# Kernel tuning notes

Hardware: AMD Instinct MI355X
Metric: run time of the kernel (lower is better)

The kernel has to match this reference:

```python
import jax, jax.numpy as jnp
import numpy as np

H = W = 64      # patch grid (shape)
WS = 8          # window_size
SHIFT = 4       # shift_size (SW-MSA)
HEAD_DIM = 32
N = WS * WS     # tokens per window


def _rel_position_index(ws):
    coords = np.stack(np.meshgrid(np.arange(ws), np.arange(ws), indexing='ij'))  # (2, ws, ws)
    cf = coords.reshape(2, -1)
    rel = cf[:, :, None] - cf[:, None, :]            # (2, N, N)
    rel = rel.transpose(1, 2, 0).astype(np.int64)    # (N, N, 2)
    rel[..., 0] += ws - 1
    rel[..., 1] += ws - 1
    rel[..., 0] *= 2 * ws - 1
    return (rel[..., 0] + rel[..., 1]).astype(np.int32)  # (N, N), values in [0,(2ws-1)^2)


def _shift_mask(h, w, ws, shift):
    # Swin cyclic-shift attention mask: (num_windows, N, N) with 0 / -100
    img = np.zeros((h, w), dtype=np.float32)
    cnt = 0
    slices = (slice(0, -ws), slice(-ws, -shift), slice(-shift, None))
    for hs in slices:
        for ws_ in slices:
            img[hs, ws_] = cnt
            cnt += 1
    win = img.reshape(h // ws, ws, w // ws, ws).transpose(0, 2, 1, 3).reshape(-1, ws * ws)
    diff = win[:, None, :] - win[:, :, None]
    return np.where(diff != 0, np.float32(-100.0), np.float32(0.0))


def setup_inputs() -> dict:
    key = jax.random.key(0)
    ks = jax.random.split(key, 6)
    dim = 384
    B = 32
    sd = 1.0 / np.sqrt(dim)
    return {
        'x': jax.random.normal(ks[0], (B, H * W, dim), jnp.float32),
        'qkv_w': jax.random.normal(ks[1], (dim, 3 * dim), jnp.float32) * sd,
        'qkv_b': jnp.zeros((3 * dim,), jnp.float32),
        'proj_w': jax.random.normal(ks[2], (dim, dim), jnp.float32) * sd,
        'proj_b': jnp.zeros((dim,), jnp.float32),
        'bias_table': jax.random.normal(ks[3], ((2 * WS - 1) ** 2, dim // HEAD_DIM), jnp.float32) * 0.02,
        'rel_index': jnp.asarray(_rel_position_index(WS)),
    }


def reference(x, qkv_w, qkv_b, proj_w, proj_b, bias_table, rel_index):
    B, L, C = x.shape
    heads = C // HEAD_DIM
    scale = HEAD_DIM ** -0.5
    nh, nw = H // WS, W // WS

    xg = x.reshape(B, H, W, C)
    if SHIFT > 0:
        xg = jnp.roll(xg, shift=(-SHIFT, -SHIFT), axis=(1, 2))

    # window partition -> (B*nWin, N, C)
    xw = xg.reshape(B, nh, WS, nw, WS, C).transpose(0, 1, 3, 2, 4, 5).reshape(B * nh * nw, N, C)

    qkv = xw @ qkv_w + qkv_b                              # (Bw, N, 3C)
    q, k, v = jnp.split(qkv, 3, axis=-1)
    def heads_first(t):
        return t.reshape(-1, N, heads, HEAD_DIM).transpose(0, 2, 1, 3)  # (Bw, h, N, d)
    q, k, v = heads_first(q), heads_first(k), heads_first(v)

    attn = jnp.einsum('bhnd,bhmd->bhnm', q * scale, k)    # (Bw, h, N, N)
    bias = bias_table[rel_index]                          # (N, N, h)
    attn = attn + bias.transpose(2, 0, 1)[None]

    if SHIFT > 0:
        mask = jnp.asarray(_shift_mask(H, W, WS, SHIFT))  # (nWin, N, N), trace-time constant
        attn = attn.reshape(B, nh * nw, heads, N, N) + mask[None, :, None]
        attn = attn.reshape(B * nh * nw, heads, N, N)

    attn = jax.nn.softmax(attn, axis=-1)
    out = jnp.einsum('bhnm,bhmd->bhnd', attn, v)          # (Bw, h, N, d)
    out = out.transpose(0, 2, 1, 3).reshape(B * nh * nw, N, C)
    out = out @ proj_w + proj_b

    # window reverse
    out = out.reshape(B, nh, nw, WS, WS, C).transpose(0, 1, 3, 2, 4, 5).reshape(B, H, W, C)
    if SHIFT > 0:
        out = jnp.roll(out, shift=(SHIFT, SHIFT), axis=(1, 2))
    return out.reshape(B, L, C)
```

## Files before the change

### kernel.cpp

```cpp
#include <hip/hip_runtime.h>
#include <hip/hip_bf16.h>

#define CDIM 384
#define NQKV 1152
#define HEADS 12
#define SHIFT_ 4
#define SCALE_Q 0.17677669529663687f

typedef __attribute__((ext_vector_type(8))) short bf16x8;
typedef __attribute__((ext_vector_type(4))) float f32x4;
typedef __attribute__((ext_vector_type(4))) float float4_t;
typedef __attribute__((ext_vector_type(4))) unsigned u32x4;
typedef __attribute__((ext_vector_type(2))) unsigned u32x2;

__device__ inline short f2bf(float f) {
    union { float f; unsigned u; } v; v.f = f;
    unsigned r = v.u + 0x7FFFu + ((v.u >> 16) & 1u);
    return (short)(r >> 16);
}

__device__ inline unsigned cvtpk(float lo, float hi) {
    unsigned r;
    asm("v_cvt_pk_bf16_f32 %0, %1, %2" : "=v"(r) : "v"(lo), "v"(hi));
    return r;
}

__device__ inline bf16x8 mk8(unsigned w0, unsigned w1, unsigned w2, unsigned w3) {
    u32x4 t = {w0, w1, w2, w3};
    return __builtin_bit_cast(bf16x8, t);
}

__device__ inline bf16x8 pack8(float4_t a, float4_t b) {
    return mk8(cvtpk(a[0], a[1]), cvtpk(a[2], a[3]),
               cvtpk(b[0], b[1]), cvtpk(b[2], b[3]));
}

__device__ inline bf16x8 regroup(unsigned p0, unsigned p1, unsigned p2,
                                 unsigned p3, int lane) {
    int lhi = (lane >> 4) & 3;
    int s0 = (lane & 15) + ((lhi & 1) ? 32 : 0);
    int s1 = s0 + 16;
    unsigned a0 = __shfl(p0, s0), b0 = __shfl(p2, s0);
    unsigned a1 = __shfl(p1, s0), b1 = __shfl(p3, s0);
    unsigned a2 = __shfl(p0, s1), b2 = __shfl(p2, s1);
    unsigned a3 = __shfl(p1, s1), b3 = __shfl(p3, s1);
    bool hi = lhi >= 2;
    return mk8(hi ? b0 : a0, hi ? b1 : a1, hi ? b2 : a2, hi ? b3 : a3);
}

__device__ inline void gl16(const short* g, const short* l) {
    __builtin_amdgcn_global_load_lds((const __attribute__((address_space(1))) void*)g,
                                     (__attribute__((address_space(3))) void*)l, 16, 0, 0);
}

__device__ inline int invswz(int c) {
    int b2 = (c >> 2) & 1, b3 = (c >> 3) & 1, b4 = (c >> 4) & 1;
    return (c & ~7) | ((b2 ^ b4) << 2) | (((((c >> 1) & 1)) ^ b3) << 1) | ((c & 1) ^ b2 ^ b4);
}

__device__ inline int region_id(int wIdx, int tok) {
    int gh = ((wIdx >> 3) << 3) + (tok >> 3);
    int gw = (wIdx & 7) * 8 + (tok & 7);
    int rh = gh < 56 ? 0 : (gh < 60 ? 1 : 2);
    int rw = gw < 56 ? 0 : (gw < 60 ? 1 : 2);
    return rh * 3 + rw;
}

__device__ inline int crow(int row) { return row * 136 + (row >> 3) * 8; }

__device__ inline size_t xrow(int mg) {
    int tok = mg & 63, win = mg >> 6;
    int b = win >> 6, wIdx = win & 63;
    int gh = ((wIdx >> 3) << 3) + (tok >> 3);
    int gw = (wIdx & 7) * 8 + (tok & 7);
    int sh_ = (gh + SHIFT_) & 63, sw_ = (gw + SHIFT_) & 63;
    return (size_t)(b * 4096 + sh_ * 64 + sw_) * CDIM;
}

__global__ void prep_kernel(const float* __restrict__ qkv_w,
                            const float* __restrict__ proj_w,
                            const float* __restrict__ bias_table,
                            const int* __restrict__ rel_index,
                            short* __restrict__ qkvwt,
                            short* __restrict__ projwt,
                            float* __restrict__ biasP) {
    int t = blockIdx.x * 256 + threadIdx.x;
    if (t < NQKV * CDIM) {
        int n = t / CDIM, k = t - n * CDIM;
        qkvwt[t] = f2bf(qkv_w[k * NQKV + n]);
    }
    if (t < CDIM * CDIM) {
        int n = t / CDIM, k = t - n * CDIM;
        projwt[t] = f2bf(proj_w[k * CDIM + n]);
    }
    if (t < HEADS * 16 * 64 * 4) {
        int r = t & 3, lane = (t >> 2) & 63, g = (t >> 8) & 15, h = t >> 12;
        int kt = g >> 2, qt = g & 3;
        int key = kt * 16 + (lane >> 4) * 4 + r;
        int query = qt * 16 + (lane & 15);
        biasP[t] = bias_table[rel_index[query * 64 + key] * HEADS + h];
    }
}

__global__ __launch_bounds__(256) void gemm_qkv(
    const float* __restrict__ x, const short* __restrict__ wt,
    const float* __restrict__ qkv_b, short* __restrict__ qkbuf,
    short* __restrict__ vT)
{
    __shared__ alignas(16) char smemb[40960];
    short* As = (short*)smemb;
    short* Bs = As + 8192;
    short* Cst = (short*)smemb;
    int tid = threadIdx.x;
    int hw = blockIdx.x;
    int lb = (hw & 7) * 1152 + (hw >> 3);
    int bm = lb / 9, bn = lb - bm * 9;
    int m0 = bm * 128, n0 = bn * 128;

    int lane = tid & 63, wv = tid >> 6;
    int c0 = wv * 128 + lane, c1 = c0 + 64;
    const float* Asrc0 = x + xrow(m0 + (c0 >> 2)) + (c0 & 3) * 8;
    const float* Asrc1 = x + xrow(m0 + (c1 >> 2)) + (c1 & 3) * 8;
    short* Aw0 = As + (c0 ^ ((c0 >> 2) & 7)) * 8;
    short* Aw1 = As + (c1 ^ ((c1 >> 2) & 7)) * 8;
    int l0 = invswz(c0), l1 = invswz(c1);
    const short* Bg0 = wt + (size_t)(n0 + (l0 >> 2)) * CDIM + (l0 & 3) * 8;
    const short* Bg1 = wt + (size_t)(n0 + (l1 >> 2)) * CDIM + (l1 & 3) * 8;
    short* Bdst0 = Bs + wv * 1024;
    short* Bdst1 = Bdst0 + 512;

    int wr = wv >> 1, wc = wv & 1;
    int lrow = lane & 15, lhi = lane >> 4;
    int arow = wr * 64 + lrow, brow = wc * 64 + lrow;
    const short* ard = As + ((((arow * 64 + lhi * 16)) ^ ((lrow & 7) << 4)) >> 1);
    const short* brd = Bs + ((((brow * 64 + lhi * 16)) ^ ((lrow & 7) << 4)) >> 1);

    f32x4 zero = {0.f, 0.f, 0.f, 0.f};
    f32x4 acc[4][4];
    #pragma unroll
    for (int i = 0; i < 4; i++)
        #pragma unroll
        for (int j = 0; j < 4; j++) acc[i][j] = zero;

    float4_t sA0[4], sA1[4];
    {
        sA0[0] = *(const float4_t*)(Asrc0);
        sA0[1] = *(const float4_t*)(Asrc0 + 4);
        sA0[2] = *(const float4_t*)(Asrc1);
        sA0[3] = *(const float4_t*)(Asrc1 + 4);
        gl16(Bg0, Bdst0);
        gl16(Bg1, Bdst1);
        gl16(Bg0 + 32, Bdst0 + 4096);
        gl16(Bg1 + 32, Bdst1 + 4096);
        *(bf16x8*)Aw0 = pack8(sA0[0], sA0[1]);
        *(bf16x8*)Aw1 = pack8(sA0[2], sA0[3]);
        sA1[0] = *(const float4_t*)(Asrc0 + 32);
        sA1[1] = *(const float4_t*)(Asrc0 + 36);
        sA1[2] = *(const float4_t*)(Asrc1 + 32);
        sA1[3] = *(const float4_t*)(Asrc1 + 36);
    }
    __builtin_amdgcn_sched_barrier(0);
    asm volatile("s_waitcnt vmcnt(6) lgkmcnt(0)");
    __builtin_amdgcn_s_barrier();
    __builtin_amdgcn_sched_barrier(0);

    #pragma unroll
    for (int ks = 0; ks < 12; ks++) {
        int curA = (ks & 1) * 4096, nxtA = 4096 - curA;
        int curB = (ks % 3) * 4096;
        if (ks < 10) {
            int k2 = (ks + 2) * 32;
            int b2 = ((ks + 2) % 3) * 4096;
            gl16(Bg0 + k2, Bdst0 + b2);
            gl16(Bg1 + k2, Bdst1 + b2);
        }
        if (ks < 11) {
            if ((ks + 1) & 1) {
                *(bf16x8*)(Aw0 + nxtA) = pack8(sA1[0], sA1[1]);
                *(bf16x8*)(Aw1 + nxtA) = pack8(sA1[2], sA1[3]);
            } else {
                *(bf16x8*)(Aw0 + nxtA) = pack8(sA0[0], sA0[1]);
                *(bf16x8*)(Aw1 + nxtA) = pack8(sA0[2], sA0[3]);
            }
        }
        if (ks < 10) {
            int k2 = (ks + 2) * 32;
            if (ks & 1) {
                sA1[0] = *(const float4_t*)(Asrc0 + k2);
                sA1[1] = *(const float4_t*)(Asrc0 + k2 + 4);
                sA1[2] = *(const float4_t*)(Asrc1 + k2);
                sA1[3] = *(const float4_t*)(Asrc1 + k2 + 4);
            } else {
                sA0[0] = *(const float4_t*)(Asrc0 + k2);
                sA0[1] = *(const float4_t*)(Asrc0 + k2 + 4);
                sA0[2] = *(const float4_t*)(Asrc1 + k2);
                sA0[3] = *(const float4_t*)(Asrc1 + k2 + 4);
            }
        }
        bf16x8 af[4], bfr[4];
        #pragma unroll
        for (int t = 0; t < 4; t++) af[t]  = *(const bf16x8*)(ard + curA + t * 512);
        #pragma unroll
        for (int t = 0; t < 4; t++) bfr[t] = *(const bf16x8*)(brd + curB + t * 512);
        __builtin_amdgcn_s_setprio(1);
        #pragma unroll
        for (int i = 0; i < 4; i++)
            #pragma unroll
            for (int j = 0; j < 4; j++)
                acc[i][j] = __builtin_amdgcn_mfma_f32_16x16x32_bf16(af[i], bfr[j], acc[i][j], 0, 0, 0);
        __builtin_amdgcn_s_setprio(0);
        __builtin_amdgcn_sched_barrier(0);
        asm volatile("s_waitcnt vmcnt(6) lgkmcnt(0)");
        __builtin_amdgcn_s_barrier();
        __builtin_amdgcn_sched_barrier(0);
    }
    #pragma unroll
    for (int tj = 0; tj < 4; tj++) {
        int col = wc * 64 + tj * 16 + lrow;
        int cg = n0 + col;
        float bias = qkv_b[cg];
        float sc = (cg < CDIM) ? SCALE_Q : 1.0f;
        #pragma unroll
        for (int ti = 0; ti < 4; ti++) {
            int row0 = wr * 64 + ti * 16 + lhi * 4;
            #pragma unroll
            for (int r = 0; r < 4; r++)
                Cst[crow(row0 + r) + col] = f2bf((acc[ti][tj][r] + bias) * sc);
        }
    }
    __syncthreads();
    if (bn < 6) {
        #pragma unroll
        for (int i = 0; i < 8; i++) {
            int rr = i * 16 + (tid >> 4);
            int cc = (tid & 15) * 8;
            bf16x8 v = *(const bf16x8*)(Cst + crow(rr) + cc);
            __builtin_nontemporal_store(v,
                (bf16x8*)(qkbuf + (size_t)(m0 + rr) * 768 + n0 + cc));
        }
    } else {
        #pragma unroll
        for (int it = 0; it < 8; it++) {
            int t = it * 256 + tid;
            int col = t >> 4, tk8 = t & 15;
            bf16x8 v;
            #pragma unroll
            for (int j = 0; j < 8; j++)
                v[j] = Cst[crow(tk8 * 8 + j) + col];
            int win = bm * 2 + (tk8 >> 3);
            int head = (bn - 6) * 4 + (col >> 5);
            int dim = col & 31;
            __builtin_nontemporal_store(v,
                (bf16x8*)(vT + (((size_t)win * HEADS + head) * 32 + dim) * 64 + (tk8 & 7) * 8));
        }
    }
}

__global__ __launch_bounds__(256) void attn_reg(
    const short* __restrict__ qkbuf, const short* __restrict__ vT,
    const float* __restrict__ biasP, short* __restrict__ attno)
{
    int tid = threadIdx.x;
    int lane = tid & 63, wv = tid >> 6;
    int lrow = lane & 15, lhi = lane >> 4;
    int task = blockIdx.x * 4 + wv;
    int w = task / 12, h = task - w * 12;
    int wIdx = w & 63;
    bool needmask = ((wIdx >> 3) == 7) || ((wIdx & 7) == 7);

    int rq[4], rk[4][4];
    #pragma unroll
    for (int qt = 0; qt < 4; qt++) rq[qt] = region_id(wIdx, qt * 16 + lrow);
    #pragma unroll
    for (int kt = 0; kt < 4; kt++)
        #pragma unroll
        for (int r = 0; r < 4; r++)
            rk[kt][r] = region_id(wIdx, kt * 16 + lhi * 4 + r);

    f32x4 zero = {0.f, 0.f, 0.f, 0.f};
    const short* qbase = qkbuf + (size_t)(w * 64) * 768;

    bf16x8 kf[4];
    #pragma unroll
    for (int kt = 0; kt < 4; kt++)
        kf[kt] = __builtin_nontemporal_load(
            (const bf16x8*)(qbase + (size_t)(kt * 16 + lrow) * 768 + CDIM + h * 32 + lhi * 8));
    bf16x8 pa[4][2];
    #pragma unroll
    for (int qt = 0; qt < 4; qt++) {
        bf16x8 qf = __builtin_nontemporal_load(
            (const bf16x8*)(qbase + (size_t)(qt * 16 + lrow) * 768 + h * 32 + lhi * 8));
        f32x4 st[4];
        __builtin_amdgcn_s_setprio(1);
        #pragma unroll
        for (int kt = 0; kt < 4; kt++)
            st[kt] = __builtin_amdgcn_mfma_f32_16x16x32_bf16(kf[kt], qf, zero, 0, 0, 0);
        __builtin_amdgcn_s_setprio(0);
        float pv[16]; float sum = 0.f;
        #pragma unroll
        for (int kt = 0; kt < 4; kt++) {
            f32x4 bb = *(const f32x4*)(biasP + (((size_t)h * 16 + kt * 4 + qt) * 64 + lane) * 4);
            #pragma unroll
            for (int r = 0; r < 4; r++) {
                float p = __expf(st[kt][r] + bb[r]);
                p = (needmask && (rq[qt] != rk[kt][r])) ? 0.f : p;
                pv[kt * 4 + r] = p; sum += p;
            }
        }
        sum += __shfl_xor(sum, 16);
        sum += __shfl_xor(sum, 32);
        float rcp = 1.0f / sum;
        unsigned a0 = cvtpk(pv[0] * rcp, pv[1] * rcp);
        unsigned a1 = cvtpk(pv[2] * rcp, pv[3] * rcp);
        unsigned a2 = cvtpk(pv[4] * rcp, pv[5] * rcp);
        unsigned a3 = cvtpk(pv[6] * rcp, pv[7] * rcp);
        pa[qt][0] = regroup(a0, a1, a2, a3, lane);
        a0 = cvtpk(pv[8] * rcp,  pv[9] * rcp);
        a1 = cvtpk(pv[10] * rcp, pv[11] * rcp);
        a2 = cvtpk(pv[12] * rcp, pv[13] * rcp);
        a3 = cvtpk(pv[14] * rcp, pv[15] * rcp);
        pa[qt][1] = regroup(a0, a1, a2, a3, lane);
    }
    const short* vb = vT + ((size_t)w * HEADS + h) * 32 * 64;
    bf16x8 vfrag[2][2];
    #pragma unroll
    for (int ks2 = 0; ks2 < 2; ks2++)
        #pragma unroll
        for (int dt = 0; dt < 2; dt++)
            vfrag[ks2][dt] = __builtin_nontemporal_load(
                (const bf16x8*)(vb + (size_t)(dt * 16 + lrow) * 64 + ks2 * 32 + lhi * 8));
    f32x4 ao2[4][2];
    #pragma unroll
    for (int qt = 0; qt < 4; qt++) { ao2[qt][0] = zero; ao2[qt][1] = zero; }
    __builtin_amdgcn_s_setprio(1);
    #pragma unroll
    for (int ks2 = 0; ks2 < 2; ks2++)
        #pragma unroll
        for (int qt = 0; qt < 4; qt++) {
            ao2[qt][0] = __builtin_amdgcn_mfma_f32_16x16x32_bf16(vfrag[ks2][0], pa[qt][ks2], ao2[qt][0], 0, 0, 0);
            ao2[qt][1] = __builtin_amdgcn_mfma_f32_16x16x32_bf16(vfrag[ks2][1], pa[qt][ks2], ao2[qt][1], 0, 0, 0);
        }
    __builtin_amdgcn_s_setprio(0);
    short* abase = attno + (size_t)(w * 64) * CDIM + h * 32 + lhi * 4;
    #pragma unroll
    for (int qt = 0; qt < 4; qt++) {
        int token = qt * 16 + lrow;
        short* p0 = abase + (size_t)token * CDIM;
        u32x2 s0, s1;
        s0[0] = cvtpk(ao2[qt][0][0], ao2[qt][0][1]);
        s0[1] = cvtpk(ao2[qt][0][2], ao2[qt][0][3]);
        s1[0] = cvtpk(ao2[qt][1][0], ao2[qt][1][1]);
        s1[1] = cvtpk(ao2[qt][1][2], ao2[qt][1][3]);
        __builtin_nontemporal_store(s0, (u32x2*)(p0));
        __builtin_nontemporal_store(s1, (u32x2*)(p0 + 16));
    }
}

__global__ __launch_bounds__(256) void gemm_proj(
    const short* __restrict__ a, const short* __restrict__ wt,
    const float* __restrict__ proj_b, float* __restrict__ out)
{
    __shared__ alignas(16) short As[8192];
    __shared__ alignas(16) short Bs[8192];
    int tid = threadIdx.x;
    int hw = blockIdx.x;
    int lb = (hw & 7) * 384 + (hw >> 3);
    int bm = lb / 3, bn = lb - bm * 3;
    int m0 = bm * 128, n0 = bn * 128;

    int lane = tid & 63, wv = tid >> 6;
    int c0 = wv * 128 + lane, c1 = c0 + 64;
    int l0 = invswz(c0), l1 = invswz(c1);
    const short* Ag0 = a + (size_t)(m0 + (l0 >> 2)) * CDIM + (l0 & 3) * 8;
    const short* Ag1 = a + (size_t)(m0 + (l1 >> 2)) * CDIM + (l1 & 3) * 8;
    const short* Bg0 = wt + (size_t)(n0 + (l0 >> 2)) * CDIM + (l0 & 3) * 8;
    const short* Bg1 = wt + (size_t)(n0 + (l1 >> 2)) * CDIM + (l1 & 3) * 8;
    short* Adst0 = As + wv * 1024;
    short* Adst1 = Adst0 + 512;
    short* Bdst0 = Bs + wv * 1024;
    short* Bdst1 = Bdst0 + 512;

    int wr = wv >> 1, wc = wv & 1;
    int lrow = lane & 15, lhi = lane >> 4;
    int arow = wr * 64 + lrow, brow = wc * 64 + lrow;
    const short* ard = As + ((((arow * 64 + lhi * 16)) ^ ((lrow & 7) << 4)) >> 1);
    const short* brd = Bs + ((((brow * 64 + lhi * 16)) ^ ((lrow & 7) << 4)) >> 1);

    f32x4 zero = {0.f, 0.f, 0.f, 0.f};
    f32x4 acc[4][4];
    #pragma unroll
    for (int i = 0; i < 4; i++)
        #pragma unroll
        for (int j = 0; j < 4; j++) acc[i][j] = zero;

    gl16(Ag0, Adst0);
    gl16(Bg0, Bdst0);
    gl16(Ag1, Adst1);
    gl16(Bg1, Bdst1);
    __syncthreads();

    #pragma unroll
    for (int ks = 0; ks < 12; ks++) {
        int cur = (ks & 1) * 4096, nxt = 4096 - cur;
        if (ks < 11) {
            int k1 = (ks + 1) * 32;
            gl16(Ag0 + k1, Adst0 + nxt);
            gl16(Bg0 + k1, Bdst0 + nxt);
            gl16(Ag1 + k1, Adst1 + nxt);
            gl16(Bg1 + k1, Bdst1 + nxt);
        }
        bf16x8 af[4], bfr[4];
        #pragma unroll
        for (int t = 0; t < 4; t++) af[t]  = *(const bf16x8*)(ard + cur + t * 512);
        #pragma unroll
        for (int t = 0; t < 4; t++) bfr[t] = *(const bf16x8*)(brd + cur + t * 512);
        __builtin_amdgcn_s_setprio(1);
        #pragma unroll
        for (int i = 0; i < 4; i++)
            #pragma unroll
            for (int j = 0; j < 4; j++)
                acc[i][j] = __builtin_amdgcn_mfma_f32_16x16x32_bf16(af[i], bfr[j], acc[i][j], 0, 0, 0);
        __builtin_amdgcn_s_setprio(0);
        __syncthreads();
    }
    #pragma unroll
    for (int ti = 0; ti < 4; ti++) {
        #pragma unroll
        for (int r = 0; r < 4; r++) {
            int m = m0 + wr * 64 + ti * 16 + lhi * 4 + r;
            int b = m >> 12, wIdx = (m >> 6) & 63, tok = m & 63;
            int gh = ((wIdx >> 3) << 3) + (tok >> 3);
            int gw = (wIdx & 7) * 8 + (tok & 7);
            int ih = (gh + SHIFT_) & 63, iw = (gw + SHIFT_) & 63;
            size_t ob = ((size_t)(b << 12) + ih * 64 + iw) * CDIM;
            #pragma unroll
            for (int tj = 0; tj < 4; tj++) {
                int col = n0 + wc * 64 + tj * 16 + lrow;
                float v = acc[ti][tj][r] + proj_b[col];
                __builtin_nontemporal_store(v, &out[ob + col]);
            }
        }
    }
}

extern "C" void kernel_launch(void* const* d_in, const int* in_sizes, int n_in,
                              void* d_out, int out_size, void* d_ws, size_t ws_size,
                              hipStream_t stream) {
    const float* x          = (const float*)d_in[0];
    const float* qkv_w      = (const float*)d_in[1];
    const float* qkv_b      = (const float*)d_in[2];
    const float* proj_w     = (const float*)d_in[3];
    const float* proj_b     = (const float*)d_in[4];
    const float* bias_table = (const float*)d_in[5];
    const int*   rel_index  = (const int*)d_in[6];
    float* out = (float*)d_out;
    char* ws = (char*)d_ws;

    short* qkvwt = (short*)(ws);
    short* projwt = (short*)(ws + 884736);
    float* biasP  = (float*)(ws + 1179648);
    short* qkbuf  = (short*)(ws + 1376256);
    short* vT     = (short*)(ws + 202702848);
    short* attno  = (short*)(ws + 303366144);

    prep_kernel<<<1728, 256, 0, stream>>>(qkv_w, proj_w, bias_table, rel_index,
                                          qkvwt, projwt, biasP);
    gemm_qkv<<<9216, 256, 0, stream>>>(x, qkvwt, qkv_b, qkbuf, vT);
    attn_reg<<<6144, 256, 0, stream>>>(qkbuf, vT, biasP, attno);
    gemm_proj<<<3072, 256, 0, stream>>>(attno, projwt, proj_b, out);
}
```

Before: 410.8 us.

## Enlarge QKV GEMM tile to 256x128 with 512-thread blocks sharing B tile

The QKV projection GEMM now uses 8 waves per block and a 256-row M tile, so each staged weight (B) tile in LDS is reused by twice as many rows. Global weight traffic per output drops, and each thread issues one B load per k-step instead of two. The epilogue runs in two passes through the shared staging buffer to fit the larger tile, with wait counts adjusted to match. LDS use rises to 56KB per block, which may limit occupancy, and the extra epilogue sync adds some serialization.

```diff
diff --git a/kernel.cpp b/kernel.cpp
--- a/kernel.cpp
+++ b/kernel.cpp
@@ -102,20 +102,20 @@
     }
 }
 
-__global__ __launch_bounds__(256) void gemm_qkv(
+__global__ __launch_bounds__(512) void gemm_qkv(
     const float* __restrict__ x, const short* __restrict__ wt,
     const float* __restrict__ qkv_b, short* __restrict__ qkbuf,
     short* __restrict__ vT)
 {
-    __shared__ alignas(16) char smemb[40960];
+    __shared__ alignas(16) char smemb[57344];
     short* As = (short*)smemb;
-    short* Bs = As + 8192;
+    short* Bs = As + 16384;
     short* Cst = (short*)smemb;
     int tid = threadIdx.x;
     int hw = blockIdx.x;
-    int lb = (hw & 7) * 1152 + (hw >> 3);
+    int lb = (hw & 7) * 576 + (hw >> 3);
     int bm = lb / 9, bn = lb - bm * 9;
-    int m0 = bm * 128, n0 = bn * 128;
+    int m0 = bm * 256, n0 = bn * 128;
 
     int lane = tid & 63, wv = tid >> 6;
     int c0 = wv * 128 + lane, c1 = c0 + 64;
@@ -123,11 +123,10 @@
     const float* Asrc1 = x + xrow(m0 + (c1 >> 2)) + (c1 & 3) * 8;
     short* Aw0 = As + (c0 ^ ((c0 >> 2) & 7)) * 8;
     short* Aw1 = As + (c1 ^ ((c1 >> 2) & 7)) * 8;
-    int l0 = invswz(c0), l1 = invswz(c1);
-    const short* Bg0 = wt + (size_t)(n0 + (l0 >> 2)) * CDIM + (l0 & 3) * 8;
-    const short* Bg1 = wt + (size_t)(n0 + (l1 >> 2)) * CDIM + (l1 & 3) * 8;
-    short* Bdst0 = Bs + wv * 1024;
-    short* Bdst1 = Bdst0 + 512;
+    int cb = wv * 64 + lane;
+    int lB = invswz(cb);
+    const short* Bg = wt + (size_t)(n0 + (lB >> 2)) * CDIM + (lB & 3) * 8;
+    short* Bdst = Bs + wv * 512;
 
     int wr = wv >> 1, wc = wv & 1;
     int lrow = lane & 15, lhi = lane >> 4;
@@ -148,10 +147,9 @@
         sA0[1] = *(const float4_t*)(Asrc0 + 4);
         sA0[2] = *(const float4_t*)(Asrc1);
         sA0[3] = *(const float4_t*)(Asrc1 + 4);
-        gl16(Bg0, Bdst0);
-        gl16(Bg1, Bdst1);
-        gl16(Bg0 + 32, Bdst0 + 4096);
-        gl16(Bg1 + 32, Bdst1 + 4096);
+        gl16(Bg, Bdst);
+        gl16(Bg + 32, Bdst + 4096);
+        __builtin_amdgcn_sched_barrier(0);
         *(bf16x8*)Aw0 = pack8(sA0[0], sA0[1]);
         *(bf16x8*)Aw1 = pack8(sA0[2], sA0[3]);
         sA1[0] = *(const float4_t*)(Asrc0 + 32);
@@ -160,19 +158,18 @@
         sA1[3] = *(const float4_t*)(Asrc1 + 36);
     }
     __builtin_amdgcn_sched_barrier(0);
-    asm volatile("s_waitcnt vmcnt(6) lgkmcnt(0)");
+    asm volatile("s_waitcnt vmcnt(5) lgkmcnt(0)");
     __builtin_amdgcn_s_barrier();
     __builtin_amdgcn_sched_barrier(0);
 
     #pragma unroll
     for (int ks = 0; ks < 12; ks++) {
-        int curA = (ks & 1) * 4096, nxtA = 4096 - curA;
+        int curA = (ks & 1) * 8192, nxtA = 8192 - curA;
         int curB = (ks % 3) * 4096;
         if (ks < 10) {
             int k2 = (ks + 2) * 32;
             int b2 = ((ks + 2) % 3) * 4096;
-            gl16(Bg0 + k2, Bdst0 + b2);
-            gl16(Bg1 + k2, Bdst1 + b2);
+            gl16(Bg + k2, Bdst + b2);
         }
         if (ks < 11) {
             if ((ks + 1) & 1) {
@@ -210,48 +207,58 @@
                 acc[i][j] = __builtin_amdgcn_mfma_f32_16x16x32_bf16(af[i], bfr[j], acc[i][j], 0, 0, 0);
         __builtin_amdgcn_s_setprio(0);
         __builtin_amdgcn_sched_barrier(0);
-        asm volatile("s_waitcnt vmcnt(6) lgkmcnt(0)");
+        if (ks < 10) {
+            asm volatile("s_waitcnt vmcnt(5) lgkmcnt(0)");
+        } else {
+            asm volatile("s_waitcnt vmcnt(0) lgkmcnt(0)");
+        }
         __builtin_amdgcn_s_barrier();
         __builtin_amdgcn_sched_barrier(0);
     }
     #pragma unroll
-    for (int tj = 0; tj < 4; tj++) {
-        int col = wc * 64 + tj * 16 + lrow;
-        int cg = n0 + col;
-        float bias = qkv_b[cg];
-        float sc = (cg < CDIM) ? SCALE_Q : 1.0f;
-        #pragma unroll
-        for (int ti = 0; ti < 4; ti++) {
-            int row0 = wr * 64 + ti * 16 + lhi * 4;
-            #pragma unroll
-            for (int r = 0; r < 4; r++)
-                Cst[crow(row0 + r) + col] = f2bf((acc[ti][tj][r] + bias) * sc);
-        }
-    }
-    __syncthreads();
-    if (bn < 6) {
-        #pragma unroll
-        for (int i = 0; i < 8; i++) {
-            int rr = i * 16 + (tid >> 4);
-            int cc = (tid & 15) * 8;
-            bf16x8 v = *(const bf16x8*)(Cst + crow(rr) + cc);
-            __builtin_nontemporal_store(v,
-                (bf16x8*)(qkbuf + (size_t)(m0 + rr) * 768 + n0 + cc));
-        }
-    } else {
-        #pragma unroll
-        for (int it = 0; it < 8; it++) {
-            int t = it * 256 + tid;
-            int col = t >> 4, tk8 = t & 15;
-            bf16x8 v;
-            #pragma unroll
-            for (int j = 0; j < 8; j++)
-                v[j] = Cst[crow(tk8 * 8 + j) + col];
-            int win = bm * 2 + (tk8 >> 3);
-            int head = (bn - 6) * 4 + (col >> 5);
-            int dim = col & 31;
-            __builtin_nontemporal_store(v,
-                (bf16x8*)(vT + (((size_t)win * HEADS + head) * 32 + dim) * 64 + (tk8 & 7) * 8));
+    for (int p = 0; p < 2; p++) {
+        if (p) __syncthreads();
+        if ((wr >> 1) == p) {
+            #pragma unroll
+            for (int tj = 0; tj < 4; tj++) {
+                int col = wc * 64 + tj * 16 + lrow;
+                int cg = n0 + col;
+                float bias = qkv_b[cg];
+                float sc = (cg < CDIM) ? SCALE_Q : 1.0f;
+                #pragma unroll
+                for (int ti = 0; ti < 4; ti++) {
+                    int row0 = (wr & 1) * 64 + ti * 16 + lhi * 4;
+                    #pragma unroll
+                    for (int r = 0; r < 4; r++)
+                        Cst[crow(row0 + r) + col] = f2bf((acc[ti][tj][r] + bias) * sc);
+                }
+            }
+        }
+        __syncthreads();
+        if (bn < 6) {
+            #pragma unroll
+            for (int i = 0; i < 4; i++) {
+                int rr = i * 32 + (tid >> 4);
+                int cc = (tid & 15) * 8;
+                bf16x8 v = *(const bf16x8*)(Cst + crow(rr) + cc);
+                __builtin_nontemporal_store(v,
+                    (bf16x8*)(qkbuf + (size_t)(m0 + p * 128 + rr) * 768 + n0 + cc));
+            }
+        } else {
+            #pragma unroll
+            for (int it = 0; it < 4; it++) {
+                int t = it * 512 + tid;
+                int col = t >> 4, tk8 = t & 15;
+                bf16x8 v;
+                #pragma unroll
+                for (int j = 0; j < 8; j++)
+                    v[j] = Cst[crow(tk8 * 8 + j) + col];
+                int win = bm * 4 + p * 2 + (tk8 >> 3);
+                int head = (bn - 6) * 4 + (col >> 5);
+                int dim = col & 31;
+                __builtin_nontemporal_store(v,
+                    (bf16x8*)(vT + (((size_t)win * HEADS + head) * 32 + dim) * 64 + (tk8 & 7) * 8));
+            }
         }
     }
 }
@@ -465,7 +472,7 @@
 
     prep_kernel<<<1728, 256, 0, stream>>>(qkv_w, proj_w, bias_table, rel_index,
                                           qkvwt, projwt, biasP);
-    gemm_qkv<<<9216, 256, 0, stream>>>(x, qkvwt, qkv_b, qkbuf, vT);
+    gemm_qkv<<<4608, 512, 0, stream>>>(x, qkvwt, qkv_b, qkbuf, vT);
     attn_reg<<<6144, 256, 0, stream>>>(qkbuf, vT, biasP, attno);
     gemm_proj<<<3072, 256, 0, stream>>>(attno, projwt, proj_b, out);
 }
```

After: 472.5 us. 1.15x slower.
